# Kernel optimization log

Measured on AMD Instinct MI355X. Metric: run time of the kernel, lower is better.

Reference implementation:

```python
import jax, jax.numpy as jnp
import numpy as np
import math

T = 2048
D_MODEL = 2048
N_H = 16
D_H = D_MODEL // N_H
EPS = 1e-5


def _rope_tables(t, d_h):
    # standard RoPE cos/sin tables, full head-dim layout matching rotate_half
    inv_freq = 1.0 / (10000.0 ** (jnp.arange(0, d_h // 2, dtype=jnp.float32) / (d_h // 2)))
    ang = jnp.arange(t, dtype=jnp.float32)[:, None] * inv_freq[None, :]  # (T, d_h/2)
    ang = jnp.concatenate([ang, ang], axis=-1)  # (T, d_h)
    return jnp.cos(ang), jnp.sin(ang)


def setup_inputs() -> dict:
    key = jax.random.key(0)
    kx, kq, kk, kv, ko = jax.random.split(key, 5)
    scale = 1.0 / math.sqrt(D_MODEL)
    cos, sin = _rope_tables(T, D_H)
    return {
        "x": jax.random.normal(kx, (T, D_MODEL), dtype=jnp.float32),
        "cos": cos,
        "sin": sin,
        "attention_mask": jnp.ones((T,), dtype=jnp.int32),
        "ln_w": jnp.ones((D_MODEL,), dtype=jnp.float32),
        "Wq": jax.random.normal(kq, (D_MODEL, D_MODEL), dtype=jnp.float32) * scale,
        "Wk": jax.random.normal(kk, (D_MODEL, D_MODEL), dtype=jnp.float32) * scale,
        "Wv": jax.random.normal(kv, (D_MODEL, D_MODEL), dtype=jnp.float32) * scale,
        "Wo": jax.random.normal(ko, (D_MODEL, D_MODEL), dtype=jnp.float32) * scale,
    }


def _rotate_half(x):
    x1, x2 = jnp.split(x, 2, axis=-1)
    return jnp.concatenate((-x2, x1), axis=-1)


def reference(x, cos, sin, attention_mask, ln_w, Wq, Wk, Wv, Wo):
    t = x.shape[0]
    # RMSNorm
    var = jnp.mean(x * x, axis=-1, keepdims=True)
    h = ln_w * x * jax.lax.rsqrt(var + EPS)
    # QKV projections (eqx Linear: weight @ x => x @ W.T), reshape to (n_h, T, d_h)
    q = (h @ Wq.T).reshape(t, N_H, D_H).transpose(1, 0, 2)
    k = (h @ Wk.T).reshape(t, N_H, D_H).transpose(1, 0, 2)
    v = (h @ Wv.T).reshape(t, N_H, D_H).transpose(1, 0, 2)
    # RoPE (cos/sin broadcast (T,d_h) -> (n_h,T,d_h))
    q = q * cos + _rotate_half(q) * sin
    k = k * cos + _rotate_half(k) * sin
    scores = jnp.einsum('hqd,hkd->hqk', q, k) / math.sqrt(D_H)
    causal = jnp.tril(jnp.ones((t, t), dtype=bool))[None]
    neg = jnp.finfo(scores.dtype).min
    am = attention_mask.astype(bool)
    allowed = causal & am[None, None, :]
    scores = jnp.where(allowed, scores, neg)
    scores = jnp.where(am[None, :, None], scores, neg)
    probs = jax.nn.softmax(scores, axis=-1)
    out = jnp.einsum('hqk,hkd->hqd', probs, v).transpose(1, 0, 2).reshape(t, -1)
    out = out @ Wo.T
    out = jnp.where(am[:, None], out, 0.0)
    return x + out
```

## Files before the change

### kernel.cpp

```cpp
#include <hip/hip_runtime.h>
#include <stdint.h>

#define TS 2048
#define DM 2048
#define NH 16
#define DH 128

typedef unsigned short u16t;
typedef __attribute__((ext_vector_type(8))) short short8;
typedef __attribute__((ext_vector_type(4))) float f32x4;
typedef __attribute__((ext_vector_type(4))) unsigned int u32x4;
typedef __attribute__((ext_vector_type(4))) unsigned short u16x4;

__device__ __forceinline__ float bf2f(u16t b) {
  return __uint_as_float(((unsigned int)b) << 16);
}
__device__ __forceinline__ u16t f2bf(float f) {
  unsigned int u = __float_as_uint(f);
  u += 0x7FFFu + ((u >> 16) & 1u);
  return (u16t)(u >> 16);
}

__device__ __forceinline__ void async_copy16(const u16t* g, u16t* l) {
  __builtin_amdgcn_global_load_lds((const __attribute__((address_space(1))) void*)g,
                                   (__attribute__((address_space(3))) void*)l, 16, 0, 0);
}

#define DPP_ROR_F(x, n) __uint_as_float(__builtin_amdgcn_update_dpp( \
    0, (int)__float_as_uint(x), 0x120 | (n), 0xF, 0xF, true))

__device__ __forceinline__ float row16_max(float x) {
  x = fmaxf(x, DPP_ROR_F(x, 8));
  x = fmaxf(x, DPP_ROR_F(x, 4));
  x = fmaxf(x, DPP_ROR_F(x, 2));
  x = fmaxf(x, DPP_ROR_F(x, 1));
  return x;
}
__device__ __forceinline__ float row16_sum(float x) {
  x += DPP_ROR_F(x, 8);
  x += DPP_ROR_F(x, 4);
  x += DPP_ROR_F(x, 2);
  x += DPP_ROR_F(x, 1);
  return x;
}

__global__ __launch_bounds__(256) void cast_rms_kernel(const float* __restrict__ W0,
                                                       const float* __restrict__ W1,
                                                       const float* __restrict__ W2,
                                                       const float* __restrict__ W3,
                                                       u16t* __restrict__ outw,
                                                       const float* __restrict__ x,
                                                       const float* __restrict__ lnw,
                                                       u16t* __restrict__ h) {
  if (blockIdx.x < 16384) {
    const int idx = blockIdx.x * 256 + threadIdx.x;
    const int mat = idx >> 20;
    const size_t off = (size_t)(idx & 0xFFFFF) * 4;
    const float* W = (mat == 0) ? W0 : (mat == 1) ? W1 : (mat == 2) ? W2 : W3;
    const f32x4 v = *(const f32x4*)(W + off);
    size_t dstoff = off;
    if (mat < 2) {
      const int row = (int)(off >> 11);
      const int col = (int)(off & 2047);
      const int d = row & 127;
      const int e = d & 63;
      const int p = ((e >> 4) * 32 + (e & 15)) + ((d >> 6) << 4);
      dstoff = ((size_t)((row & ~127) | p) << 11) | (size_t)col;
    }
    union { u16t s[4]; uint64_t u; } o;
#pragma unroll
    for (int i = 0; i < 4; ++i) o.s[i] = f2bf(v[i]);
    *(uint64_t*)(outw + (size_t)mat * (DM * DM) + dstoff) = o.u;
    return;
  }
  const int row = blockIdx.x - 16384;
  const int tid = threadIdx.x;
  const float* xr = x + (size_t)row * DM + tid * 8;
  f32x4 v0 = *(const f32x4*)(xr);
  f32x4 v1 = *(const f32x4*)(xr + 4);
  float f[8];
#pragma unroll
  for (int i = 0; i < 4; ++i) { f[i] = v0[i]; f[i + 4] = v1[i]; }
  float ss = 0.f;
#pragma unroll
  for (int i = 0; i < 8; ++i) ss += f[i] * f[i];
#pragma unroll
  for (int off = 1; off < 64; off <<= 1) ss += __shfl_xor(ss, off, 64);
  __shared__ float wsum[4];
  if ((tid & 63) == 0) wsum[tid >> 6] = ss;
  __syncthreads();
  float tot = wsum[0] + wsum[1] + wsum[2] + wsum[3];
  float rs = rsqrtf(tot * (1.0f / DM) + 1e-5f);
  f32x4 w0 = *(const f32x4*)(lnw + tid * 8);
  f32x4 w1 = *(const f32x4*)(lnw + tid * 8 + 4);
  u32x4 o;
#pragma unroll
  for (int i = 0; i < 4; ++i) {
    unsigned int lo = f2bf(f[2 * i]     * ((2 * i     < 4) ? w0[2 * i]     : w1[2 * i - 4]) * rs);
    unsigned int hi = f2bf(f[2 * i + 1] * ((2 * i + 1 < 4) ? w0[2 * i + 1] : w1[2 * i - 3]) * rs);
    o[i] = lo | (hi << 16);
  }
  *(u32x4*)(h + (size_t)row * DM + tid * 8) = o;
}

__global__ __launch_bounds__(512, 2) void gemm_qkv(
    const u16t* __restrict__ A,
    const u16t* __restrict__ B0, const u16t* __restrict__ B1, const u16t* __restrict__ B2,
    u16t* __restrict__ Cq, u16t* __restrict__ Ck, u16t* __restrict__ Cv,
    const float* __restrict__ cosb, const float* __restrict__ sinb) {
  __shared__ u16t Ab[2][128 * 64];
  __shared__ u16t Bb[3][2][128 * 64];
  const int tid  = threadIdx.x;
  const int wave = tid >> 6;
  const int lane = tid & 63;
  const int quad = lane >> 4;
  const int c16  = lane & 15;
  const int h7   = c16 & 7;
  const int wm   = wave >> 2;
  const int wn   = wave & 3;
  const int bid  = blockIdx.x;
  const int wgid = (bid & 7) * 32 + (bid >> 3);
  const int m0   = (wgid & 15) * 128;
  const int n0   = (wgid >> 4) * 128;

  const int srow = lane >> 3;
  const int sg   = (lane & 7) ^ srow;
  auto stage = [&](int d, int k0) {
    const size_t koff = (size_t)k0 + sg * 8;
#pragma unroll
    for (int c = 0; c < 2; ++c) {
      const int rb = wave * 16 + c * 8;
      async_copy16(A  + (size_t)(m0 + rb + srow) * DM + koff, &Ab[d][rb * 64]);
      async_copy16(B0 + (size_t)(n0 + rb + srow) * DM + koff, &Bb[0][d][rb * 64]);
      async_copy16(B1 + (size_t)(n0 + rb + srow) * DM + koff, &Bb[1][d][rb * 64]);
      async_copy16(B2 + (size_t)(n0 + rb + srow) * DM + koff, &Bb[2][d][rb * 64]);
    }
  };

  const f32x4 fzero = {0.f, 0.f, 0.f, 0.f};
  f32x4 acc[3][4][2];
#pragma unroll
  for (int m = 0; m < 3; ++m)
#pragma unroll
    for (int i = 0; i < 4; ++i)
#pragma unroll
      for (int j = 0; j < 2; ++j) acc[m][i][j] = fzero;

  stage(0, 0);
  asm volatile("s_waitcnt vmcnt(0)" ::: "memory");
  __builtin_amdgcn_s_barrier();

  for (int kt = 0; kt < DM / 64; ++kt) {
    const int cur = kt & 1;
    if (kt + 1 < DM / 64) stage(cur ^ 1, (kt + 1) * 64);
    const u16t* Abuf = Ab[cur];
    __builtin_amdgcn_s_setprio(1);
#pragma unroll
    for (int ks = 0; ks < 2; ++ks) {
      const int gsw = ((ks * 4 + quad) ^ h7) * 8;
      short8 af[4], bfr[3][2];
#pragma unroll
      for (int i = 0; i < 4; ++i)
        af[i] = *(const short8*)(Abuf + (wm * 64 + i * 16 + c16) * 64 + gsw);
#pragma unroll
      for (int m = 0; m < 3; ++m)
#pragma unroll
        for (int nt = 0; nt < 2; ++nt)
          bfr[m][nt] = *(const short8*)(&Bb[m][cur][0] + (wn * 32 + nt * 16 + c16) * 64 + gsw);
#pragma unroll
      for (int m = 0; m < 3; ++m)
#pragma unroll
        for (int i = 0; i < 4; ++i)
#pragma unroll
          for (int nt = 0; nt < 2; ++nt)
            acc[m][i][nt] =
                __builtin_amdgcn_mfma_f32_16x16x32_bf16(af[i], bfr[m][nt], acc[m][i][nt], 0, 0, 0);
    }
    __builtin_amdgcn_s_setprio(0);
    asm volatile("s_waitcnt vmcnt(0)" ::: "memory");
    __builtin_amdgcn_s_barrier();
  }

#pragma unroll
  for (int mat = 0; mat < 2; ++mat) {
    u16t* C = mat ? Ck : Cq;
#pragma unroll
    for (int mt = 0; mt < 4; ++mt) {
#pragma unroll
      for (int r = 0; r < 4; ++r) {
        const int row = m0 + wm * 64 + mt * 16 + quad * 4 + r;
        const size_t base = (size_t)row * DM;
        const int col = n0 + wn * 32 + c16;
        const int p = col & 127;
        const int dorig = ((p >> 5) << 4) + c16;
        const float cv = cosb[row * DH + dorig];
        const float sv = sinb[row * DH + dorig];
        const float x1 = acc[mat][mt][0][r];
        const float x2 = acc[mat][mt][1][r];
        C[base + col]      = f2bf(x1 * cv - x2 * sv);
        C[base + col + 16] = f2bf(x2 * cv + x1 * sv);
      }
    }
  }
#pragma unroll
  for (int mt = 0; mt < 4; ++mt) {
#pragma unroll
    for (int r = 0; r < 4; ++r) {
      const int row = m0 + wm * 64 + mt * 16 + quad * 4 + r;
#pragma unroll
      for (int nt = 0; nt < 2; ++nt) {
        const int col = n0 + wn * 32 + nt * 16 + c16;
        Cv[(size_t)col * TS + row] = f2bf(acc[2][mt][nt][r]);
      }
    }
  }
}

__global__ __launch_bounds__(512, 2) void gemm_out(
    const u16t* __restrict__ A, const u16t* __restrict__ B0,
    const float* __restrict__ xres, const int* __restrict__ am,
    float* __restrict__ out) {
  __shared__ u16t Ab[2][128 * 64];
  __shared__ u16t Bb[2][128 * 64];
  const int tid  = threadIdx.x;
  const int wave = tid >> 6;
  const int lane = tid & 63;
  const int quad = lane >> 4;
  const int c16  = lane & 15;
  const int h7   = c16 & 7;
  const int wm   = wave >> 2;
  const int wn   = wave & 3;
  const int bid  = blockIdx.x;
  const int wgid = (bid & 7) * 32 + (bid >> 3);
  const int m0   = (wgid & 15) * 128;
  const int n0   = (wgid >> 4) * 128;

  const int srow = lane >> 3;
  const int sg   = (lane & 7) ^ srow;
  auto stage = [&](int d, int k0) {
    const size_t koff = (size_t)k0 + sg * 8;
#pragma unroll
    for (int c = 0; c < 2; ++c) {
      const int rb = wave * 16 + c * 8;
      async_copy16(A  + (size_t)(m0 + rb + srow) * DM + koff, &Ab[d][rb * 64]);
      async_copy16(B0 + (size_t)(n0 + rb + srow) * DM + koff, &Bb[d][rb * 64]);
    }
  };

  const f32x4 fzero = {0.f, 0.f, 0.f, 0.f};
  f32x4 acc[4][2];
#pragma unroll
  for (int i = 0; i < 4; ++i)
#pragma unroll
    for (int j = 0; j < 2; ++j) acc[i][j] = fzero;

  stage(0, 0);
  asm volatile("s_waitcnt vmcnt(0)" ::: "memory");
  __builtin_amdgcn_s_barrier();

  for (int kt = 0; kt < DM / 64; ++kt) {
    const int cur = kt & 1;
    if (kt + 1 < DM / 64) stage(cur ^ 1, (kt + 1) * 64);
    const u16t* Abuf = Ab[cur];
    const u16t* Bbuf = Bb[cur];
    __builtin_amdgcn_s_setprio(1);
#pragma unroll
    for (int ks = 0; ks < 2; ++ks) {
      const int gsw = ((ks * 4 + quad) ^ h7) * 8;
      short8 af[4], bfr[2];
#pragma unroll
      for (int i = 0; i < 4; ++i)
        af[i] = *(const short8*)(Abuf + (wm * 64 + i * 16 + c16) * 64 + gsw);
#pragma unroll
      for (int nt = 0; nt < 2; ++nt)
        bfr[nt] = *(const short8*)(Bbuf + (wn * 32 + nt * 16 + c16) * 64 + gsw);
#pragma unroll
      for (int i = 0; i < 4; ++i)
#pragma unroll
        for (int nt = 0; nt < 2; ++nt)
          acc[i][nt] =
              __builtin_amdgcn_mfma_f32_16x16x32_bf16(af[i], bfr[nt], acc[i][nt], 0, 0, 0);
    }
    __builtin_amdgcn_s_setprio(0);
    asm volatile("s_waitcnt vmcnt(0)" ::: "memory");
    __builtin_amdgcn_s_barrier();
  }

#pragma unroll
  for (int mt = 0; mt < 4; ++mt) {
#pragma unroll
    for (int r = 0; r < 4; ++r) {
      const int row = m0 + wm * 64 + mt * 16 + quad * 4 + r;
      const float mk = (am[row] != 0) ? 1.f : 0.f;
      const size_t base = (size_t)row * DM;
#pragma unroll
      for (int nt = 0; nt < 2; ++nt) {
        const int col = n0 + wn * 32 + nt * 16 + c16;
        out[base + col] = xres[base + col] + mk * acc[mt][nt][r];
      }
    }
  }
}

__global__ __launch_bounds__(256) void attn_kernel(const u16t* __restrict__ Q,
                                                   const u16t* __restrict__ K,
                                                   const u16t* __restrict__ Vt,
                                                   const int* __restrict__ am,
                                                   u16t* __restrict__ O) {
  __shared__ u16t Klds[128 * 128];
  __shared__ u16t Vlds[128 * 128];
  __shared__ u16t Plds[4][2048];
  const int wave = threadIdx.x >> 6;
  const int lane = threadIdx.x & 63;
  const int x    = blockIdx.x;
  const int half = x >> 8;
  const int idx  = x & 255;
  const int head = idx & (NH - 1);
  const int grp  = idx >> 4;
  const int qt   = half ? grp : (TS / 64 - 1 - grp);
  const int q0   = qt * 64 + wave * 16;
  const int quad = lane >> 4;
  const int c16  = lane & 15;
  const u16t* Qh  = Q + head * DH;
  const u16t* Kh  = K + head * DH;
  const u16t* Vth = Vt + (size_t)head * DH * TS;
  u16t* Pw = Plds[wave];

  const int row_s = (lane >> 4);
  const int g_s   = (lane & 15);

  short8 qf[4];
#pragma unroll
  for (int dc = 0; dc < 4; ++dc)
    qf[dc] = *(const short8*)(Qh + (size_t)(q0 + c16) * DM + dc * 32 + quad * 8);

  const f32x4 fzero = {0.f, 0.f, 0.f, 0.f};
  float m_run[4], l_run[4];
  f32x4 o_acc[8];
#pragma unroll
  for (int r = 0; r < 4; ++r) { m_run[r] = -1e30f; l_run[r] = 0.f; }
#pragma unroll
  for (int nt = 0; nt < 8; ++nt) o_acc[nt] = fzero;

  const float scale = 0.08838834764831845f;
  const int ntiles = (qt * 64 + 191) >> 7;

  for (int kt = 0; kt < ntiles; ++kt) {
    const int k0 = kt * 128;
    __syncthreads();
#pragma unroll
    for (int c = 0; c < 8; ++c) {
      const int ch = wave * 8 + c;
      const int r  = 4 * ch + row_s;
      const int g  = g_s ^ (r & 15);
      async_copy16(Kh + (size_t)(k0 + r) * DM + g * 8, Klds + ch * 512);
      async_copy16(Vth + (size_t)r * TS + k0 + g * 8, Vlds + ch * 512);
    }
    __syncthreads();

    f32x4 s[8];
#pragma unroll
    for (int ns = 0; ns < 8; ++ns) {
      f32x4 sa = fzero;
      const int rr = ns * 16 + c16;
#pragma unroll
      for (int dc = 0; dc < 4; ++dc) {
        short8 kf = *(const short8*)(Klds + rr * 128 + (((dc * 4 + quad) ^ c16) * 8));
        sa = __builtin_amdgcn_mfma_f32_16x16x32_bf16(qf[dc], kf, sa, 0, 0, 0);
      }
      s[ns] = sa;
    }

    float pv[8][4], tmax[4];
#pragma unroll
    for (int r = 0; r < 4; ++r) tmax[r] = -1e30f;
#pragma unroll
    for (int ns = 0; ns < 8; ++ns) {
      const int key = k0 + ns * 16 + c16;
      const bool kok = (am[key] != 0);
#pragma unroll
      for (int r = 0; r < 4; ++r) {
        const int qrow = q0 + quad * 4 + r;
        float v = s[ns][r] * scale;
        if (key > qrow || !kok) v = -1e30f;
        pv[ns][r] = v;
        tmax[r] = fmaxf(tmax[r], v);
      }
    }
    float alpha[4], rsum[4];
#pragma unroll
    for (int r = 0; r < 4; ++r) {
      const float mn = fmaxf(m_run[r], row16_max(tmax[r]));
      alpha[r] = __expf(m_run[r] - mn);
      m_run[r] = mn;
      float rs = 0.f;
#pragma unroll
      for (int ns = 0; ns < 8; ++ns) {
        const float e = __expf(pv[ns][r] - mn);
        pv[ns][r] = e;
        rs += e;
      }
      rsum[r] = row16_sum(rs);
      l_run[r] = l_run[r] * alpha[r] + rsum[r];
    }

#pragma unroll
    for (int ns = 0; ns < 8; ++ns)
#pragma unroll
      for (int r = 0; r < 4; ++r)
        Pw[(ns >> 1) * 512 + (quad * 4 + r) * 32 + (ns & 1) * 16 + c16] = f2bf(pv[ns][r]);
    asm volatile("s_waitcnt lgkmcnt(0)" ::: "memory");
    short8 pf[4];
#pragma unroll
    for (int c = 0; c < 4; ++c)
      pf[c] = *(const short8*)(Pw + c * 512 + c16 * 32 + quad * 8);

#pragma unroll
    for (int nt = 0; nt < 8; ++nt)
#pragma unroll
      for (int r = 0; r < 4; ++r) o_acc[nt][r] *= alpha[r];
#pragma unroll
    for (int nt = 0; nt < 8; ++nt) {
      const int rr = nt * 16 + c16;
#pragma unroll
      for (int c = 0; c < 4; ++c) {
        short8 vf = *(const short8*)(Vlds + rr * 128 + (((c * 4 + quad) ^ c16) * 8));
        o_acc[nt] = __builtin_amdgcn_mfma_f32_16x16x32_bf16(pf[c], vf, o_acc[nt], 0, 0, 0);
      }
    }
  }

#pragma unroll
  for (int r = 0; r < 4; ++r) {
    const float inv = 1.0f / fmaxf(l_run[r], 1e-20f);
    const int qrow = q0 + quad * 4 + r;
#pragma unroll
    for (int nt = 0; nt < 8; ++nt)
      O[(size_t)qrow * DM + head * DH + nt * 16 + c16] = f2bf(o_acc[nt][r] * inv);
  }
}

extern "C" void kernel_launch(void* const* d_in, const int* in_sizes, int n_in,
                              void* d_out, int out_size, void* d_ws, size_t ws_size,
                              hipStream_t stream) {
  const float* x    = (const float*)d_in[0];
  const float* cosb = (const float*)d_in[1];
  const float* sinb = (const float*)d_in[2];
  const int*   am   = (const int*)d_in[3];
  const float* lnw  = (const float*)d_in[4];
  const float* Wq   = (const float*)d_in[5];
  const float* Wk   = (const float*)d_in[6];
  const float* Wv   = (const float*)d_in[7];
  const float* Wo   = (const float*)d_in[8];
  float* out = (float*)d_out;

  u16t* h    = (u16t*)d_ws;
  u16t* Q    = h + (size_t)TS * DM;
  u16t* K    = Q + (size_t)TS * DM;
  u16t* Vt   = K + (size_t)TS * DM;
  u16t* attn = Vt + (size_t)TS * DM;
  u16t* Wb   = attn + (size_t)TS * DM;
  u16t* Wqb = Wb;
  u16t* Wkb = Wb + (size_t)DM * DM;
  u16t* Wvb = Wb + 2 * (size_t)DM * DM;
  u16t* Wob = Wb + 3 * (size_t)DM * DM;

  cast_rms_kernel<<<16384 + TS, 256, 0, stream>>>(Wq, Wk, Wv, Wo, Wb, x, lnw, h);
  gemm_qkv<<<256, 512, 0, stream>>>(h, Wqb, Wkb, Wvb, Q, K, Vt, cosb, sinb);
  attn_kernel<<<NH * (TS / 64), 256, 0, stream>>>(Q, K, Vt, am, attn);
  gemm_out<<<256, 512, 0, stream>>>(attn, Wob, x, am, out);
}
```

Baseline: 283.5 us.

## Transpose attention MFMA operands so softmax rows live per lane

Swaps the A/B operands of both MFMAs so that S^T and O^T are computed. Each lane then owns one query row, so the running max and sum become scalars, reduced with two cross-quad shuffles instead of DPP row reductions over four rows. P is packed with v_cvt_pk_bf16_f32 into a swizzled LDS layout, and the mask is loaded as an int4 vector. The output goes through LDS so the global stores are coalesced 16-byte writes. The cost is extra LDS traffic for the output staging and new swizzle logic that must stay correct.

```diff
diff --git a/kernel.cpp b/kernel.cpp
--- a/kernel.cpp
+++ b/kernel.cpp
@@ -10,7 +10,7 @@
 typedef __attribute__((ext_vector_type(8))) short short8;
 typedef __attribute__((ext_vector_type(4))) float f32x4;
 typedef __attribute__((ext_vector_type(4))) unsigned int u32x4;
-typedef __attribute__((ext_vector_type(4))) unsigned short u16x4;
+typedef __attribute__((ext_vector_type(4))) int i32x4;
 
 __device__ __forceinline__ float bf2f(u16t b) {
   return __uint_as_float(((unsigned int)b) << 16);
@@ -24,24 +24,6 @@
 __device__ __forceinline__ void async_copy16(const u16t* g, u16t* l) {
   __builtin_amdgcn_global_load_lds((const __attribute__((address_space(1))) void*)g,
                                    (__attribute__((address_space(3))) void*)l, 16, 0, 0);
-}
-
-#define DPP_ROR_F(x, n) __uint_as_float(__builtin_amdgcn_update_dpp( \
-    0, (int)__float_as_uint(x), 0x120 | (n), 0xF, 0xF, true))
-
-__device__ __forceinline__ float row16_max(float x) {
-  x = fmaxf(x, DPP_ROR_F(x, 8));
-  x = fmaxf(x, DPP_ROR_F(x, 4));
-  x = fmaxf(x, DPP_ROR_F(x, 2));
-  x = fmaxf(x, DPP_ROR_F(x, 1));
-  return x;
-}
-__device__ __forceinline__ float row16_sum(float x) {
-  x += DPP_ROR_F(x, 8);
-  x += DPP_ROR_F(x, 4);
-  x += DPP_ROR_F(x, 2);
-  x += DPP_ROR_F(x, 1);
-  return x;
 }
 
 __global__ __launch_bounds__(256) void cast_rms_kernel(const float* __restrict__ W0,
@@ -325,6 +307,8 @@
   const u16t* Kh  = K + head * DH;
   const u16t* Vth = Vt + (size_t)head * DH * TS;
   u16t* Pw = Plds[wave];
+  uint32_t* Pw32 = (uint32_t*)Pw;
+  const int pswz = (c16 & 7) << 2;
 
   const int row_s = (lane >> 4);
   const int g_s   = (lane & 15);
@@ -335,15 +319,14 @@
     qf[dc] = *(const short8*)(Qh + (size_t)(q0 + c16) * DM + dc * 32 + quad * 8);
 
   const f32x4 fzero = {0.f, 0.f, 0.f, 0.f};
-  float m_run[4], l_run[4];
+  float m_run = -1e30f, l_run = 0.f;
   f32x4 o_acc[8];
 #pragma unroll
-  for (int r = 0; r < 4; ++r) { m_run[r] = -1e30f; l_run[r] = 0.f; }
-#pragma unroll
-  for (int nt = 0; nt < 8; ++nt) o_acc[nt] = fzero;
+  for (int mt = 0; mt < 8; ++mt) o_acc[mt] = fzero;
 
   const float scale = 0.08838834764831845f;
   const int ntiles = (qt * 64 + 191) >> 7;
+  const int qrow = q0 + c16;
 
   for (int kt = 0; kt < ntiles; ++kt) {
     const int k0 = kt * 128;
@@ -366,77 +349,87 @@
 #pragma unroll
       for (int dc = 0; dc < 4; ++dc) {
         short8 kf = *(const short8*)(Klds + rr * 128 + (((dc * 4 + quad) ^ c16) * 8));
-        sa = __builtin_amdgcn_mfma_f32_16x16x32_bf16(qf[dc], kf, sa, 0, 0, 0);
+        sa = __builtin_amdgcn_mfma_f32_16x16x32_bf16(kf, qf[dc], sa, 0, 0, 0);
       }
       s[ns] = sa;
     }
 
-    float pv[8][4], tmax[4];
-#pragma unroll
-    for (int r = 0; r < 4; ++r) tmax[r] = -1e30f;
+    float pv[8][4];
+    float tmax = -1e30f;
 #pragma unroll
     for (int ns = 0; ns < 8; ++ns) {
-      const int key = k0 + ns * 16 + c16;
-      const bool kok = (am[key] != 0);
+      const i32x4 a4 = *(const i32x4*)(am + k0 + ns * 16 + quad * 4);
 #pragma unroll
       for (int r = 0; r < 4; ++r) {
-        const int qrow = q0 + quad * 4 + r;
+        const int key = k0 + ns * 16 + quad * 4 + r;
         float v = s[ns][r] * scale;
-        if (key > qrow || !kok) v = -1e30f;
+        if (key > qrow || a4[r] == 0) v = -1e30f;
         pv[ns][r] = v;
-        tmax[r] = fmaxf(tmax[r], v);
-      }
-    }
-    float alpha[4], rsum[4];
-#pragma unroll
-    for (int r = 0; r < 4; ++r) {
-      const float mn = fmaxf(m_run[r], row16_max(tmax[r]));
-      alpha[r] = __expf(m_run[r] - mn);
-      m_run[r] = mn;
-      float rs = 0.f;
-#pragma unroll
-      for (int ns = 0; ns < 8; ++ns) {
+        tmax = fmaxf(tmax, v);
+      }
+    }
+    tmax = fmaxf(tmax, __shfl_xor(tmax, 16, 64));
+    tmax = fmaxf(tmax, __shfl_xor(tmax, 32, 64));
+    const float mn = fmaxf(m_run, tmax);
+    const float alpha = __expf(m_run - mn);
+    m_run = mn;
+    float rs = 0.f;
+#pragma unroll
+    for (int ns = 0; ns < 8; ++ns)
+#pragma unroll
+      for (int r = 0; r < 4; ++r) {
         const float e = __expf(pv[ns][r] - mn);
         pv[ns][r] = e;
         rs += e;
       }
-      rsum[r] = row16_sum(rs);
-      l_run[r] = l_run[r] * alpha[r] + rsum[r];
-    }
+    rs += __shfl_xor(rs, 16, 64);
+    rs += __shfl_xor(rs, 32, 64);
+    l_run = l_run * alpha + rs;
 
 #pragma unroll
     for (int ns = 0; ns < 8; ++ns)
 #pragma unroll
-      for (int r = 0; r < 4; ++r)
-        Pw[(ns >> 1) * 512 + (quad * 4 + r) * 32 + (ns & 1) * 16 + c16] = f2bf(pv[ns][r]);
+      for (int i = 0; i < 2; ++i) {
+        uint32_t pk;
+        asm("v_cvt_pk_bf16_f32 %0, %1, %2"
+            : "=v"(pk) : "v"(pv[ns][2 * i]), "v"(pv[ns][2 * i + 1]));
+        Pw32[c16 * 64 + ((ns * 8 + quad * 2 + i) ^ pswz)] = pk;
+      }
     asm volatile("s_waitcnt lgkmcnt(0)" ::: "memory");
-    short8 pf[4];
-#pragma unroll
-    for (int c = 0; c < 4; ++c)
-      pf[c] = *(const short8*)(Pw + c * 512 + c16 * 32 + quad * 8);
-
-#pragma unroll
-    for (int nt = 0; nt < 8; ++nt)
-#pragma unroll
-      for (int r = 0; r < 4; ++r) o_acc[nt][r] *= alpha[r];
-#pragma unroll
-    for (int nt = 0; nt < 8; ++nt) {
-      const int rr = nt * 16 + c16;
-#pragma unroll
-      for (int c = 0; c < 4; ++c) {
-        short8 vf = *(const short8*)(Vlds + rr * 128 + (((c * 4 + quad) ^ c16) * 8));
-        o_acc[nt] = __builtin_amdgcn_mfma_f32_16x16x32_bf16(pf[c], vf, o_acc[nt], 0, 0, 0);
-      }
-    }
-  }
-
-#pragma unroll
-  for (int r = 0; r < 4; ++r) {
-    const float inv = 1.0f / fmaxf(l_run[r], 1e-20f);
-    const int qrow = q0 + quad * 4 + r;
-#pragma unroll
-    for (int nt = 0; nt < 8; ++nt)
-      O[(size_t)qrow * DM + head * DH + nt * 16 + c16] = f2bf(o_acc[nt][r] * inv);
+    short8 pa[4];
+#pragma unroll
+    for (int kb = 0; kb < 4; ++kb)
+      pa[kb] = *(const short8*)(Pw32 + c16 * 64 + ((kb * 16 + quad * 4) ^ pswz));
+
+#pragma unroll
+    for (int mt = 0; mt < 8; ++mt)
+#pragma unroll
+      for (int r = 0; r < 4; ++r) o_acc[mt][r] *= alpha;
+#pragma unroll
+    for (int mt = 0; mt < 8; ++mt) {
+      const int rrv = mt * 16 + c16;
+#pragma unroll
+      for (int kb = 0; kb < 4; ++kb) {
+        short8 vf = *(const short8*)(Vlds + rrv * 128 + (((kb * 4 + quad) ^ c16) * 8));
+        o_acc[mt] = __builtin_amdgcn_mfma_f32_16x16x32_bf16(vf, pa[kb], o_acc[mt], 0, 0, 0);
+      }
+    }
+  }
+
+  const float inv = 1.0f / fmaxf(l_run, 1e-20f);
+#pragma unroll
+  for (int mt = 0; mt < 8; ++mt)
+#pragma unroll
+    for (int r = 0; r < 4; ++r) {
+      const int d = mt * 16 + quad * 4 + r;
+      Pw[c16 * 128 + d] = f2bf(o_acc[mt][r] * inv);
+    }
+  asm volatile("s_waitcnt lgkmcnt(0)" ::: "memory");
+#pragma unroll
+  for (int p = 0; p < 4; ++p) {
+    const int row = p * 4 + quad;
+    short8 v = *(const short8*)(Pw + row * 128 + c16 * 8);
+    *(short8*)(O + (size_t)(q0 + row) * DM + head * DH + c16 * 8) = v;
   }
 }
 
```

After: 280.4 us. No clear change (-1.1%).
